# Kernel optimization log

Measured on AMD Instinct MI355X. Metric: run time of the kernel, lower is better.

Reference implementation:

```python
import jax, jax.numpy as jnp
import numpy as np

N_NODES = 50000
N_EDGES = 800000
NODE_DIM = 64
MSG_DIM = 64
EDGE_DIM = 4
ROUNDS = 2


def setup_inputs() -> dict:
    key = jax.random.key(0)
    ks = jax.random.split(key, 10)
    in_dim = 2 * NODE_DIM + EDGE_DIM  # cat([src hv, dst hv, he])
    return {
        "hv": jax.random.normal(ks[0], (N_NODES, NODE_DIM), dtype=jnp.float32),
        "he": jax.random.uniform(ks[1], (N_EDGES, EDGE_DIM), dtype=jnp.float32),
        "W_msg": jax.random.normal(ks[2], (ROUNDS, in_dim, MSG_DIM), dtype=jnp.float32) * 0.05,
        "b_msg": jax.random.normal(ks[3], (ROUNDS, MSG_DIM), dtype=jnp.float32) * 0.05,
        "W_ih": jax.random.normal(ks[4], (ROUNDS, MSG_DIM, 3 * NODE_DIM), dtype=jnp.float32) * 0.05,
        "W_hh": jax.random.normal(ks[5], (ROUNDS, NODE_DIM, 3 * NODE_DIM), dtype=jnp.float32) * 0.05,
        "b_ih": jax.random.normal(ks[6], (ROUNDS, 3 * NODE_DIM), dtype=jnp.float32) * 0.05,
        "b_hh": jax.random.normal(ks[7], (ROUNDS, 3 * NODE_DIM), dtype=jnp.float32) * 0.05,
        "src": jax.random.randint(ks[8], (N_EDGES,), 0, N_NODES, dtype=jnp.int64)
        if jax.config.jax_enable_x64 else jax.random.randint(ks[8], (N_EDGES,), 0, N_NODES).astype(jnp.int32),
        "dst": jax.random.randint(ks[9], (N_EDGES,), 0, N_NODES).astype(jnp.int32),
    }


def gru_cell(a, h, W_ih, W_hh, b_ih, b_hh):
    # torch.nn.GRUCell math; gate order (r, z, n) along the 3H axis
    gi = a @ W_ih + b_ih   # [N, 3H]
    gh = h @ W_hh + b_hh   # [N, 3H]
    i_r, i_z, i_n = jnp.split(gi, 3, axis=1)
    h_r, h_z, h_n = jnp.split(gh, 3, axis=1)
    r = jax.nn.sigmoid(i_r + h_r)
    z = jax.nn.sigmoid(i_z + h_z)
    n = jnp.tanh(i_n + r * h_n)
    return (1.0 - z) * n + z * h


def reference(hv, he, W_msg, b_msg, W_ih, W_hh, b_ih, b_hh, src, dst):
    # GraphProp.forward: per-round gather -> message MLP -> scatter-sum -> GRU update
    N = hv.shape[0]
    src = src.astype(jnp.int32)
    dst = dst.astype(jnp.int32)
    rounds = W_msg.shape[0]
    for t in range(rounds):
        # dgmg_msg: m = cat([src hv, dst hv, he])  [E, 2*D+E_dim]
        m_in = jnp.concatenate([hv[src], hv[dst], he], axis=1)
        msg = m_in @ W_msg[t] + b_msg[t]  # message_funcs[t] (Linear + Identity)
        # dgmg_reduce: sum of inbound messages per destination node
        a = jax.ops.segment_sum(msg, dst, num_segments=N)  # [N, MSG_DIM]
        hv = gru_cell(a, hv, W_ih[t], W_hh[t], b_ih[t], b_hh[t])
    return hv
```

## Files before the change

kernel.cpp:

```cpp
#include <hip/hip_runtime.h>

#define N_NODES 50000
#define N_EDGES 800000
#define D 64
#define EDIM 4
#define IN_DIM 132
#define H3 192
#define XS 65

typedef unsigned short ushort;
typedef __attribute__((ext_vector_type(8))) unsigned short ushort8_t;

__device__ __forceinline__ float bf2f(ushort u) {
    union { unsigned int i; float f; } x;
    x.i = ((unsigned int)u) << 16;
    return x.f;
}
__device__ __forceinline__ ushort f2bf(float f) {
    union { float f; unsigned int i; } x;
    x.f = f;
    unsigned int r = x.i + 0x7FFFu + ((x.i >> 16) & 1u);
    return (ushort)(r >> 16);
}


__global__ void k_count(const int* __restrict__ dst, int* __restrict__ deg) {
    int e = blockIdx.x * blockDim.x + threadIdx.x;
    if (e < N_EDGES) atomicAdd(&deg[dst[e]], 1);
}

__global__ __launch_bounds__(256) void k_scan1(const int* __restrict__ deg,
                                               int* __restrict__ offsets,
                                               int* __restrict__ bsum) {
    __shared__ int sm[256];
    int tid = threadIdx.x;
    int i = blockIdx.x * 256 + tid;
    int x = (i < N_NODES) ? deg[i] : 0;
    sm[tid] = x;
    __syncthreads();
    for (int s = 1; s < 256; s <<= 1) {
        int v = (tid >= s) ? sm[tid - s] : 0;
        __syncthreads();
        sm[tid] += v;
        __syncthreads();
    }
    if (i < N_NODES) offsets[i] = sm[tid] - x;
    if (tid == 255) bsum[blockIdx.x] = sm[255];
}

__global__ __launch_bounds__(256) void k_scan2(const int* __restrict__ bsum,
                                               int* __restrict__ boff, int nblk) {
    __shared__ int sm[256];
    int tid = threadIdx.x;
    int x = (tid < nblk) ? bsum[tid] : 0;
    sm[tid] = x;
    __syncthreads();
    for (int s = 1; s < 256; s <<= 1) {
        int v = (tid >= s) ? sm[tid - s] : 0;
        __syncthreads();
        sm[tid] += v;
        __syncthreads();
    }
    if (tid < nblk) boff[tid] = sm[tid] - x;
}

__global__ __launch_bounds__(256) void k_scan3(int* __restrict__ offsets,
                                               const int* __restrict__ boff) {
    int i = blockIdx.x * 256 + threadIdx.x;
    if (i < N_NODES) offsets[i] += boff[blockIdx.x];
}

__global__ void k_fill(const int* __restrict__ src, const int* __restrict__ dst,
                       const int* __restrict__ offsets, int* __restrict__ cursor,
                       int* __restrict__ csr_src, int* __restrict__ csr_eid) {
    int e = blockIdx.x * blockDim.x + threadIdx.x;
    if (e < N_EDGES) {
        int d = dst[e];
        int pos = offsets[d] + atomicAdd(&cursor[d], 1);
        csr_src[pos] = src[e];
        csr_eid[pos] = e;
    }
}

__global__ __launch_bounds__(256) void k_prep(const float* __restrict__ hv,
                                              ushort* __restrict__ hvb) {
    int i = blockIdx.x * blockDim.x + threadIdx.x;
    if (i >= (N_NODES * D) / 8) return;
    const float4* p = (const float4*)(hv + (size_t)i * 8);
    float4 a = p[0], b = p[1];
    ushort8_t o;
    o[0] = f2bf(a.x); o[1] = f2bf(a.y); o[2] = f2bf(a.z); o[3] = f2bf(a.w);
    o[4] = f2bf(b.x); o[5] = f2bf(b.y); o[6] = f2bf(b.z); o[7] = f2bf(b.w);
    *(ushort8_t*)(hvb + (size_t)i * 8) = o;
}


template <int ROUND>
__global__ __launch_bounds__(512) void k_fused(const float* __restrict__ hv_in,
                                               const ushort* __restrict__ hvb_in,
                                               ushort* __restrict__ hvb_out,
                                               const float* __restrict__ he,
                                               const int* __restrict__ csr_src,
                                               const int* __restrict__ csr_eid,
                                               const int* __restrict__ offsets,
                                               const int* __restrict__ deg,
                                               float* __restrict__ Hsum,
                                               const float* __restrict__ W_msg,
                                               const float* __restrict__ b_msg,
                                               const float* __restrict__ W_ih,
                                               const float* __restrict__ W_hh,
                                               const float* __restrict__ b_ih,
                                               const float* __restrict__ b_hh,
                                               float* __restrict__ hv_out) {
    __shared__ float XT[IN_DIM * XS];

    const int tid = threadIdx.x;
    const int n_base = blockIdx.x * D;
    const int lane = tid & 63;

    {
        int nl = tid >> 3;
        int c8 = tid & 7;
        int n = n_base + nl;
        if (n >= N_NODES) n = N_NODES - 1;
        const float4* Hp = (const float4*)(hv_in + (size_t)n * D);
        float4 h0 = Hp[c8 * 2], h1 = Hp[c8 * 2 + 1];
        int k0 = c8 * 8;
        XT[(64 + k0 + 0) * XS + nl] = h0.x; XT[(64 + k0 + 1) * XS + nl] = h0.y;
        XT[(64 + k0 + 2) * XS + nl] = h0.z; XT[(64 + k0 + 3) * XS + nl] = h0.w;
        XT[(64 + k0 + 4) * XS + nl] = h1.x; XT[(64 + k0 + 5) * XS + nl] = h1.y;
        XT[(64 + k0 + 6) * XS + nl] = h1.z; XT[(64 + k0 + 7) * XS + nl] = h1.w;
        if (ROUND != 0 && c8 == 0) {
            float4 hs = *(const float4*)(Hsum + (size_t)n * EDIM);
            XT[128 * XS + nl] = hs.x; XT[129 * XS + nl] = hs.y;
            XT[130 * XS + nl] = hs.z; XT[131 * XS + nl] = hs.w;
        }
    }

    {
        const int w8 = (tid >> 6) * 8;
        const int g = lane >> 3;
        const int c = lane & 7;
        for (int q = 0; q < 8; ++q) {
            const int nl = w8 + q;
            int n = n_base + nl;
            const bool nv = (n < N_NODES);
            if (!nv) n = N_NODES - 1;
            const int off = offsets[n];
            const int cnt = deg[n];
            float acc[8];
#pragma unroll
            for (int i = 0; i < 8; ++i) acc[i] = 0.f;
            float4 hacc = make_float4(0.f, 0.f, 0.f, 0.f);
            for (int e = g; e < cnt; e += 8) {
                int sn = csr_src[off + e];
                ushort8_t v = *(const ushort8_t*)(hvb_in + (size_t)sn * D + c * 8);
#pragma unroll
                for (int i = 0; i < 8; ++i) acc[i] += bf2f(v[i]);
                if (ROUND == 0 && c == 0) {
                    int eid = csr_eid[off + e];
                    float4 h = *(const float4*)(he + (size_t)eid * EDIM);
                    hacc.x += h.x; hacc.y += h.y; hacc.z += h.z; hacc.w += h.w;
                }
            }
#pragma unroll
            for (int m = 8; m <= 32; m <<= 1)
#pragma unroll
                for (int i = 0; i < 8; ++i) acc[i] += __shfl_xor(acc[i], m);
            if (g == 0) {
#pragma unroll
                for (int i = 0; i < 8; ++i) XT[(c * 8 + i) * XS + nl] = acc[i];
            }
            if (ROUND == 0) {
#pragma unroll
                for (int m = 8; m <= 32; m <<= 1) {
                    hacc.x += __shfl_xor(hacc.x, m); hacc.y += __shfl_xor(hacc.y, m);
                    hacc.z += __shfl_xor(hacc.z, m); hacc.w += __shfl_xor(hacc.w, m);
                }
                if (lane == 0) {
                    XT[128 * XS + nl] = hacc.x; XT[129 * XS + nl] = hacc.y;
                    XT[130 * XS + nl] = hacc.z; XT[131 * XS + nl] = hacc.w;
                    if (nv) *(float4*)(Hsum + (size_t)n * EDIM) = hacc;
                }
            }
        }
    }
    __syncthreads();

    const int w = __builtin_amdgcn_readfirstlane(tid) >> 6;
    const int jb = w * 8;
    const int n = n_base + lane;
    const bool nvalid = (n < N_NODES);
    const int nc = nvalid ? n : N_NODES - 1;
    const float degf = (float)deg[nc];

    const float* __restrict__ Wm = W_msg + (size_t)ROUND * IN_DIM * D;

    float acc1[8], acc2[8];
#pragma unroll
    for (int i = 0; i < 8; ++i) { acc1[i] = 0.f; acc2[i] = 0.f; }

#pragma unroll 4
    for (int k = 0; k < 64; ++k) {
        float aS = XT[k * XS + lane];
        float aH = XT[(64 + k) * XS + lane];
        const float* wr1 = Wm + k * D + jb;
        const float* wr2 = Wm + (64 + k) * D + jb;
#pragma unroll
        for (int i = 0; i < 8; ++i) {
            acc1[i] = fmaf(aS, wr1[i], acc1[i]);
            acc2[i] = fmaf(aH, wr2[i], acc2[i]);
        }
    }
#pragma unroll
    for (int q = 0; q < 4; ++q) {
        float aQ = XT[(128 + q) * XS + lane];
        const float* wr = Wm + (128 + q) * D + jb;
#pragma unroll
        for (int i = 0; i < 8; ++i) acc1[i] = fmaf(aQ, wr[i], acc1[i]);
    }

    const float* bmp = b_msg + (size_t)ROUND * D + jb;
    float av[8];
#pragma unroll
    for (int i = 0; i < 8; ++i) av[i] = acc1[i] + degf * (acc2[i] + bmp[i]);

    __syncthreads();
#pragma unroll
    for (int i = 0; i < 8; ++i) XT[(jb + i) * XS + lane] = av[i];
    __syncthreads();

    const float* __restrict__ Wi = W_ih + (size_t)ROUND * D * H3;
    const float* __restrict__ Wh = W_hh + (size_t)ROUND * D * H3;
    const float* bi = b_ih + (size_t)ROUND * H3;
    const float* bh = b_hh + (size_t)ROUND * H3;

    float aR[8], aZ[8], aN[8], aHN[8];
#pragma unroll
    for (int i = 0; i < 8; ++i) {
        aR[i] = bi[jb + i] + bh[jb + i];
        aZ[i] = bi[64 + jb + i] + bh[64 + jb + i];
        aN[i] = bi[128 + jb + i];
        aHN[i] = bh[128 + jb + i];
    }

#pragma unroll 4
    for (int k = 0; k < 64; ++k) {
        float Aa = XT[k * XS + lane];
        const float* wr = Wi + k * H3;
#pragma unroll
        for (int i = 0; i < 8; ++i) {
            aR[i] = fmaf(Aa, wr[jb + i], aR[i]);
            aZ[i] = fmaf(Aa, wr[64 + jb + i], aZ[i]);
            aN[i] = fmaf(Aa, wr[128 + jb + i], aN[i]);
        }
    }
#pragma unroll 4
    for (int k = 0; k < 64; ++k) {
        float Ah = XT[(64 + k) * XS + lane];
        const float* wr = Wh + k * H3;
#pragma unroll
        for (int i = 0; i < 8; ++i) {
            aR[i] = fmaf(Ah, wr[jb + i], aR[i]);
            aZ[i] = fmaf(Ah, wr[64 + jb + i], aZ[i]);
            aHN[i] = fmaf(Ah, wr[128 + jb + i], aHN[i]);
        }
    }

    float o[8];
#pragma unroll
    for (int i = 0; i < 8; ++i) {
        float r = 1.f / (1.f + __expf(-aR[i]));
        float z = 1.f / (1.f + __expf(-aZ[i]));
        float nin = aN[i] + r * aHN[i];
        float nn = 2.f / (1.f + __expf(-2.f * nin)) - 1.f;
        float hold = XT[(64 + jb + i) * XS + lane];
        o[i] = (1.f - z) * nn + z * hold;
    }
    if (nvalid) {
        float4* op = (float4*)(hv_out + (size_t)n * D + jb);
        op[0] = make_float4(o[0], o[1], o[2], o[3]);
        op[1] = make_float4(o[4], o[5], o[6], o[7]);
        if (ROUND == 0) {
            ushort8_t ob;
#pragma unroll
            for (int i = 0; i < 8; ++i) ob[i] = f2bf(o[i]);
            *(ushort8_t*)(hvb_out + (size_t)n * D + jb) = ob;
        }
    }
}


extern "C" void kernel_launch(void* const* d_in, const int* in_sizes, int n_in,
                              void* d_out, int out_size, void* d_ws, size_t ws_size,
                              hipStream_t stream) {
    const float* hv = (const float*)d_in[0];
    const float* he = (const float*)d_in[1];
    const float* W_msg = (const float*)d_in[2];
    const float* b_msg = (const float*)d_in[3];
    const float* W_ih = (const float*)d_in[4];
    const float* W_hh = (const float*)d_in[5];
    const float* b_ih = (const float*)d_in[6];
    const float* b_hh = (const float*)d_in[7];
    const int* src = (const int*)d_in[8];
    const int* dst = (const int*)d_in[9];
    float* out = (float*)d_out;

    char* p = (char*)d_ws;
    int* deg = (int*)p;        p += (size_t)N_NODES * sizeof(int);
    int* cursor = (int*)p;     p += (size_t)N_NODES * sizeof(int);
    int* offsets = (int*)p;    p += (size_t)N_NODES * sizeof(int);
    int* bsum = (int*)p;       p += 256 * sizeof(int);
    int* boff = (int*)p;       p += 256 * sizeof(int);
    int* csr_src = (int*)p;    p += (size_t)N_EDGES * sizeof(int);
    int* csr_eid = (int*)p;    p += (size_t)N_EDGES * sizeof(int);
    float* Hsum = (float*)p;   p += (size_t)N_NODES * EDIM * sizeof(float);
    float* hv_buf = (float*)p; p += (size_t)N_NODES * D * sizeof(float);
    ushort* hvb_A = (ushort*)p; p += (size_t)N_NODES * D * sizeof(ushort);
    ushort* hvb_B = (ushort*)p; p += (size_t)N_NODES * D * sizeof(ushort);

    const int NBLK = (N_NODES + 255) / 256;

    hipMemsetAsync(deg, 0, N_NODES * sizeof(int), stream);
    hipMemsetAsync(cursor, 0, N_NODES * sizeof(int), stream);

    k_count<<<(N_EDGES + 255) / 256, 256, 0, stream>>>(dst, deg);
    k_scan1<<<NBLK, 256, 0, stream>>>(deg, offsets, bsum);
    k_scan2<<<1, 256, 0, stream>>>(bsum, boff, NBLK);
    k_scan3<<<NBLK, 256, 0, stream>>>(offsets, boff);
    k_fill<<<(N_EDGES + 255) / 256, 256, 0, stream>>>(src, dst, offsets, cursor, csr_src, csr_eid);
    k_prep<<<(N_NODES * D / 8 + 255) / 256, 256, 0, stream>>>(hv, hvb_A);

    const int GBLK = (N_NODES + 63) / 64;

    k_fused<0><<<GBLK, 512, 0, stream>>>(hv, hvb_A, hvb_B, he, csr_src, csr_eid, offsets,
                                         deg, Hsum, W_msg, b_msg, W_ih, W_hh, b_ih, b_hh,
                                         hv_buf);

    k_fused<1><<<GBLK, 512, 0, stream>>>(hv_buf, hvb_B, (ushort*)nullptr, he, csr_src,
                                         csr_eid, offsets, deg, Hsum, W_msg, b_msg, W_ih,
                                         W_hh, b_ih, b_hh, out);
}
```

Baseline: 428.5 us.

## Move edge-feature sum to atomic kernel and gather one feature per lane

Edge-feature sums per destination are now computed by a separate atomic-add kernel over edges instead of inside the round-0 gather, so csr_eid no longer has to be built or read. The neighbor gather changes from 8 edge groups of 8 lanes each loading 16 bytes to a full wavefront reading one bf16 per lane per edge, with eight source indices loaded per iteration and no cross-lane reductions. This removes shuffle reductions and eid traffic, but issues 2-byte loads per lane and serialises the edges of each node within a wave. Float atomics also make the Hsum summation order nondeterministic.

```diff
diff --git a/kernel.cpp b/kernel.cpp
--- a/kernel.cpp
+++ b/kernel.cpp
@@ -72,13 +72,25 @@
 
 __global__ void k_fill(const int* __restrict__ src, const int* __restrict__ dst,
                        const int* __restrict__ offsets, int* __restrict__ cursor,
-                       int* __restrict__ csr_src, int* __restrict__ csr_eid) {
+                       int* __restrict__ csr_src) {
     int e = blockIdx.x * blockDim.x + threadIdx.x;
     if (e < N_EDGES) {
         int d = dst[e];
         int pos = offsets[d] + atomicAdd(&cursor[d], 1);
         csr_src[pos] = src[e];
-        csr_eid[pos] = e;
+    }
+}
+
+__global__ void k_hsum(const float* __restrict__ he, const int* __restrict__ dst,
+                       float* __restrict__ Hsum) {
+    int e = blockIdx.x * blockDim.x + threadIdx.x;
+    if (e < N_EDGES) {
+        int d = dst[e];
+        float4 h = *(const float4*)(he + (size_t)e * EDIM);
+        atomicAdd(&Hsum[d * 4 + 0], h.x);
+        atomicAdd(&Hsum[d * 4 + 1], h.y);
+        atomicAdd(&Hsum[d * 4 + 2], h.z);
+        atomicAdd(&Hsum[d * 4 + 3], h.w);
     }
 }
 
@@ -99,12 +111,10 @@
 __global__ __launch_bounds__(512) void k_fused(const float* __restrict__ hv_in,
                                                const ushort* __restrict__ hvb_in,
                                                ushort* __restrict__ hvb_out,
-                                               const float* __restrict__ he,
                                                const int* __restrict__ csr_src,
-                                               const int* __restrict__ csr_eid,
                                                const int* __restrict__ offsets,
                                                const int* __restrict__ deg,
-                                               float* __restrict__ Hsum,
+                                               const float* __restrict__ Hsum,
                                                const float* __restrict__ W_msg,
                                                const float* __restrict__ b_msg,
                                                const float* __restrict__ W_ih,
@@ -130,7 +140,7 @@
         XT[(64 + k0 + 2) * XS + nl] = h0.z; XT[(64 + k0 + 3) * XS + nl] = h0.w;
         XT[(64 + k0 + 4) * XS + nl] = h1.x; XT[(64 + k0 + 5) * XS + nl] = h1.y;
         XT[(64 + k0 + 6) * XS + nl] = h1.z; XT[(64 + k0 + 7) * XS + nl] = h1.w;
-        if (ROUND != 0 && c8 == 0) {
+        if (c8 == 0) {
             float4 hs = *(const float4*)(Hsum + (size_t)n * EDIM);
             XT[128 * XS + nl] = hs.x; XT[129 * XS + nl] = hs.y;
             XT[130 * XS + nl] = hs.z; XT[131 * XS + nl] = hs.w;
@@ -138,51 +148,39 @@
     }
 
     {
-        const int w8 = (tid >> 6) * 8;
-        const int g = lane >> 3;
-        const int c = lane & 7;
+        const int w8 = (tid >> 6) << 3;
         for (int q = 0; q < 8; ++q) {
             const int nl = w8 + q;
             int n = n_base + nl;
-            const bool nv = (n < N_NODES);
-            if (!nv) n = N_NODES - 1;
-            const int off = offsets[n];
-            const int cnt = deg[n];
-            float acc[8];
-#pragma unroll
-            for (int i = 0; i < 8; ++i) acc[i] = 0.f;
-            float4 hacc = make_float4(0.f, 0.f, 0.f, 0.f);
-            for (int e = g; e < cnt; e += 8) {
-                int sn = csr_src[off + e];
-                ushort8_t v = *(const ushort8_t*)(hvb_in + (size_t)sn * D + c * 8);
-#pragma unroll
-                for (int i = 0; i < 8; ++i) acc[i] += bf2f(v[i]);
-                if (ROUND == 0 && c == 0) {
-                    int eid = csr_eid[off + e];
-                    float4 h = *(const float4*)(he + (size_t)eid * EDIM);
-                    hacc.x += h.x; hacc.y += h.y; hacc.z += h.z; hacc.w += h.w;
-                }
+            if (n >= N_NODES) n = N_NODES - 1;
+            const int off = __builtin_amdgcn_readfirstlane(offsets[n]);
+            const int cnt = __builtin_amdgcn_readfirstlane(deg[n]);
+            float acc = 0.f;
+            int e = 0;
+            for (; e + 8 <= cnt; e += 8) {
+                int s0 = csr_src[off + e + 0];
+                int s1 = csr_src[off + e + 1];
+                int s2 = csr_src[off + e + 2];
+                int s3 = csr_src[off + e + 3];
+                int s4 = csr_src[off + e + 4];
+                int s5 = csr_src[off + e + 5];
+                int s6 = csr_src[off + e + 6];
+                int s7 = csr_src[off + e + 7];
+                float v0 = bf2f(hvb_in[(size_t)s0 * D + lane]);
+                float v1 = bf2f(hvb_in[(size_t)s1 * D + lane]);
+                float v2 = bf2f(hvb_in[(size_t)s2 * D + lane]);
+                float v3 = bf2f(hvb_in[(size_t)s3 * D + lane]);
+                float v4 = bf2f(hvb_in[(size_t)s4 * D + lane]);
+                float v5 = bf2f(hvb_in[(size_t)s5 * D + lane]);
+                float v6 = bf2f(hvb_in[(size_t)s6 * D + lane]);
+                float v7 = bf2f(hvb_in[(size_t)s7 * D + lane]);
+                acc += ((v0 + v1) + (v2 + v3)) + ((v4 + v5) + (v6 + v7));
             }
-#pragma unroll
-            for (int m = 8; m <= 32; m <<= 1)
-#pragma unroll
-                for (int i = 0; i < 8; ++i) acc[i] += __shfl_xor(acc[i], m);
-            if (g == 0) {
-#pragma unroll
-                for (int i = 0; i < 8; ++i) XT[(c * 8 + i) * XS + nl] = acc[i];
+            for (; e < cnt; ++e) {
+                int s = csr_src[off + e];
+                acc += bf2f(hvb_in[(size_t)s * D + lane]);
             }
-            if (ROUND == 0) {
-#pragma unroll
-                for (int m = 8; m <= 32; m <<= 1) {
-                    hacc.x += __shfl_xor(hacc.x, m); hacc.y += __shfl_xor(hacc.y, m);
-                    hacc.z += __shfl_xor(hacc.z, m); hacc.w += __shfl_xor(hacc.w, m);
-                }
-                if (lane == 0) {
-                    XT[128 * XS + nl] = hacc.x; XT[129 * XS + nl] = hacc.y;
-                    XT[130 * XS + nl] = hacc.z; XT[131 * XS + nl] = hacc.w;
-                    if (nv) *(float4*)(Hsum + (size_t)n * EDIM) = hacc;
-                }
-            }
+            XT[lane * XS + nl] = acc;
         }
     }
     __syncthreads();
@@ -313,7 +311,6 @@
     int* bsum = (int*)p;       p += 256 * sizeof(int);
     int* boff = (int*)p;       p += 256 * sizeof(int);
     int* csr_src = (int*)p;    p += (size_t)N_EDGES * sizeof(int);
-    int* csr_eid = (int*)p;    p += (size_t)N_EDGES * sizeof(int);
     float* Hsum = (float*)p;   p += (size_t)N_NODES * EDIM * sizeof(float);
     float* hv_buf = (float*)p; p += (size_t)N_NODES * D * sizeof(float);
     ushort* hvb_A = (ushort*)p; p += (size_t)N_NODES * D * sizeof(ushort);
@@ -323,21 +320,22 @@
 
     hipMemsetAsync(deg, 0, N_NODES * sizeof(int), stream);
     hipMemsetAsync(cursor, 0, N_NODES * sizeof(int), stream);
+    hipMemsetAsync(Hsum, 0, (size_t)N_NODES * EDIM * sizeof(float), stream);
 
     k_count<<<(N_EDGES + 255) / 256, 256, 0, stream>>>(dst, deg);
     k_scan1<<<NBLK, 256, 0, stream>>>(deg, offsets, bsum);
     k_scan2<<<1, 256, 0, stream>>>(bsum, boff, NBLK);
     k_scan3<<<NBLK, 256, 0, stream>>>(offsets, boff);
-    k_fill<<<(N_EDGES + 255) / 256, 256, 0, stream>>>(src, dst, offsets, cursor, csr_src, csr_eid);
+    k_fill<<<(N_EDGES + 255) / 256, 256, 0, stream>>>(src, dst, offsets, cursor, csr_src);
+    k_hsum<<<(N_EDGES + 255) / 256, 256, 0, stream>>>(he, dst, Hsum);
     k_prep<<<(N_NODES * D / 8 + 255) / 256, 256, 0, stream>>>(hv, hvb_A);
 
     const int GBLK = (N_NODES + 63) / 64;
 
-    k_fused<0><<<GBLK, 512, 0, stream>>>(hv, hvb_A, hvb_B, he, csr_src, csr_eid, offsets,
+    k_fused<0><<<GBLK, 512, 0, stream>>>(hv, hvb_A, hvb_B, csr_src, offsets, deg, Hsum,
+                                         W_msg, b_msg, W_ih, W_hh, b_ih, b_hh, hv_buf);
+
+    k_fused<1><<<GBLK, 512, 0, stream>>>(hv_buf, hvb_B, (ushort*)nullptr, csr_src, offsets,
                                          deg, Hsum, W_msg, b_msg, W_ih, W_hh, b_ih, b_hh,
-                                         hv_buf);
-
-    k_fused<1><<<GBLK, 512, 0, stream>>>(hv_buf, hvb_B, (ushort*)nullptr, he, csr_src,
-                                         csr_eid, offsets, deg, Hsum, W_msg, b_msg, W_ih,
-                                         W_hh, b_ih, b_hh, out);
-}
+                                         out);
+}
```

Measured after the change: 550.7 us. 1.29x slower.
